# Optimization experiments

Measured on AMD Instinct MI355X. Metric: run time of the kernel, lower is better.

Reference implementation:

```python
import jax, jax.numpy as jnp
import numpy as np

B, N_PER, H, EMB, V, S, L = 128, 205, 200, 768, 50265, 512, 6
N = B * N_PER

def conv1d(x, w, b, pad):
    # x: [B, Cin, L], w: [Cout, Cin, K]
    out = jax.lax.conv_general_dilated(x, w, (1,), [(pad, pad)],
                                       dimension_numbers=('NCH', 'OIH', 'NCH'))
    return out + b[None, :, None]

def setup_inputs() -> dict:
    key = jax.random.key(0)
    ks = jax.random.split(key, 24)
    s = lambda fan: 1.0 / np.sqrt(fan)
    inp = {
        'x': jax.random.normal(ks[0], (N, H), jnp.float32),
        'edge_index': jax.random.randint(ks[1], (2, 209920), 0, N, jnp.int32),
        'input_ids': jax.random.randint(ks[2], (B, S), 0, V, jnp.int32),
        'embed_table': jax.random.normal(ks[3], (V, EMB), jnp.float32) * 0.02,
        'ggc_w': jax.random.normal(ks[4], (L, H, H), jnp.float32) * s(H),
        'gru_wih': jax.random.normal(ks[5], (3 * H, H), jnp.float32) * s(H),
        'gru_whh': jax.random.normal(ks[6], (3 * H, H), jnp.float32) * s(H),
        'gru_bih': jnp.zeros((3 * H,), jnp.float32),
        'gru_bhh': jnp.zeros((3 * H,), jnp.float32),
        'conv0_w': jax.random.normal(ks[7], (200, 200, 3), jnp.float32) * s(200 * 3),
        'conv0_b': jnp.zeros((200,), jnp.float32),
        'conv1_w': jax.random.normal(ks[8], (200, EMB, 3), jnp.float32) * s(EMB * 3),
        'conv1_b': jnp.zeros((200,), jnp.float32),
        'conv2_w': jax.random.normal(ks[9], (200, EMB, 4), jnp.float32) * s(EMB * 4),
        'conv2_b': jnp.zeros((200,), jnp.float32),
        'conv3_w': jax.random.normal(ks[10], (200, EMB, 5), jnp.float32) * s(EMB * 5),
        'conv3_b': jnp.zeros((200,), jnp.float32),
        'fc1_w': jax.random.normal(ks[11], (256, 800), jnp.float32) * s(800),
        'fc1_b': jnp.zeros((256,), jnp.float32),
        'fc2_w': jax.random.normal(ks[12], (128, 256), jnp.float32) * s(256),
        'fc2_b': jnp.zeros((128,), jnp.float32),
        'fc3_w': jax.random.normal(ks[13], (2, 128), jnp.float32) * s(128),
        'fc3_b': jnp.zeros((2,), jnp.float32),
    }
    return inp

def gated_graph_conv(x, edge_index, ggc_w, wih, whh, bih, bhh):
    src, dst = edge_index[0], edge_index[1]
    h = x  # [N, H], in_dim == out_channels so no padding needed
    for i in range(L):
        m = h @ ggc_w[i]                                   # [N, H]
        agg = jax.ops.segment_sum(m[src], dst, num_segments=N)  # scatter-add at targets
        gi = agg @ wih.T + bih                             # [N, 3H]
        gh = h @ whh.T + bhh
        ir, iz, inn = jnp.split(gi, 3, axis=1)
        hr, hz, hn = jnp.split(gh, 3, axis=1)
        r = jax.nn.sigmoid(ir + hr)
        z = jax.nn.sigmoid(iz + hz)
        n = jnp.tanh(inn + r * hn)
        h = (1.0 - z) * n + z * h
    return h

def reference(x, edge_index, input_ids, embed_table, ggc_w, gru_wih, gru_whh,
              gru_bih, gru_bhh, conv0_w, conv0_b, conv1_w, conv1_b, conv2_w,
              conv2_b, conv3_w, conv3_b, fc1_w, fc1_b, fc2_w, fc2_b, fc3_w, fc3_b):
    g = gated_graph_conv(x, edge_index, ggc_w, gru_wih, gru_whh, gru_bih, gru_bhh)
    g = g.reshape(B, N_PER, H).transpose(0, 2, 1)          # [B, 200, N_PER]
    e = embed_table[input_ids].transpose(0, 2, 1)          # [B, 768, S]
    x0 = jax.nn.relu(conv1d(g, conv0_w, conv0_b, 1))
    x1 = jax.nn.relu(conv1d(e, conv1_w, conv1_b, 0))
    x2 = jax.nn.relu(conv1d(e, conv2_w, conv2_b, 0))
    x3 = jax.nn.relu(conv1d(e, conv3_w, conv3_b, 0))
    feats = jnp.concatenate([x0.max(axis=2), x1.max(axis=2),
                             x2.max(axis=2), x3.max(axis=2)], axis=1)  # [B, 800]
    h = jax.nn.relu(feats @ fc1_w.T + fc1_b)   # dropout is identity in eval
    h = jax.nn.relu(h @ fc2_w.T + fc2_b)
    return h @ fc3_w.T + fc3_b                 # [B, 2]
```

## Files before the change

kernel.cpp:

```cpp
#include <hip/hip_runtime.h>
#include <math.h>

namespace {

constexpr int NB    = 128;
constexpr int NPER  = 205;
constexpr int H     = 200;
constexpr int EMBD  = 768;
constexpr int SEQ   = 512;
constexpr int NLAY  = 6;
constexpr int NNODE = NB * NPER;
constexpr int NEDGE = 209920;

typedef __bf16 bf16;
typedef _Float16 f16;
typedef __attribute__((ext_vector_type(8))) __bf16 bf16x8;
typedef __attribute__((ext_vector_type(8))) _Float16 f16x8;
typedef __attribute__((ext_vector_type(4))) float f32x4;
typedef unsigned short ushort8 __attribute__((ext_vector_type(8)));
typedef float float4v __attribute__((ext_vector_type(4)));

__device__ __forceinline__ float sigm(float x) { return 1.0f / (1.0f + expf(-x)); }

__device__ __forceinline__ unsigned short f2bf(float x) {
    unsigned int u = __float_as_uint(x);
    unsigned int r = (u + 0x7fffu + ((u >> 16) & 1u)) >> 16;
    return (unsigned short)r;
}
__device__ __forceinline__ unsigned short f2h(float x) {
    union { f16 h; unsigned short u; } c;
    c.h = (f16)x;
    return c.u;
}
__device__ __forceinline__ float h2f(unsigned short u) {
    union { unsigned short u; f16 h; } c;
    c.u = u;
    return (float)c.h;
}

__device__ __forceinline__ int pk_unit(int row, int s) {
    int q = row >> 1;
    return q * 8 + ((((row & 1) << 2) | s) ^ (q & 7));
}

template<bool BIAS, bool OUTF16>
__global__ __launch_bounds__(256, 4)
void gemm_w64(const unsigned short* __restrict__ A, int lda,
              const unsigned short* __restrict__ B,
              const float* __restrict__ bias, int Mreal, int Nreal,
              float* __restrict__ Cf, unsigned short* __restrict__ Ch,
              int ldc, int Kpad)
{
    __shared__ unsigned short As[128 * 64];
    __shared__ unsigned short Bs[128 * 64];

    const int p0 = blockIdx.x * 128;
    const int o0 = blockIdx.y * 128;
    const int tid = threadIdx.x, lane = tid & 63, wid = tid >> 6;
    const int wm = wid >> 1, wn = wid & 1;
    const int lrow = lane & 15, lk = lane >> 4;

    f32x4 acc[4][4];
    #pragma unroll
    for (int i = 0; i < 4; ++i)
        #pragma unroll
        for (int j = 0; j < 4; ++j) acc[i][j] = (f32x4){0.f, 0.f, 0.f, 0.f};

    for (int c0 = 0; c0 < Kpad; c0 += 64) {
        __syncthreads();
        for (int i = wid; i < 32; i += 4) {
            if (i < 16) {
                int u = i * 64 + lane;
                int row = u >> 3, slot = u & 7;
                int ss = slot ^ (row & 7);
                const unsigned short* sA = A + (size_t)(p0 + row) * lda + c0 + ss * 8;
                __builtin_amdgcn_global_load_lds(
                    (const __attribute__((address_space(1))) void*)sA,
                    (__attribute__((address_space(3))) void*)(As + i * 512), 16, 0, 0);
            } else {
                int i2 = i - 16;
                int u = i2 * 64 + lane;
                int row = u >> 3, slot = u & 7;
                int ss = slot ^ (row & 7);
                const unsigned short* sB = B + (size_t)(o0 + row) * Kpad + c0 + ss * 8;
                __builtin_amdgcn_global_load_lds(
                    (const __attribute__((address_space(1))) void*)sB,
                    (__attribute__((address_space(3))) void*)(Bs + i2 * 512), 16, 0, 0);
            }
        }
        __syncthreads();
        #pragma unroll
        for (int hf = 0; hf < 2; ++hf) {
            f16x8 vb[4];
            #pragma unroll
            for (int fn = 0; fn < 4; ++fn) {
                int r = wn * 64 + fn * 16 + lrow;
                int sl = (hf * 4 + lk) ^ (r & 7);
                vb[fn] = *reinterpret_cast<const f16x8*>(&Bs[r * 64 + sl * 8]);
            }
            #pragma unroll
            for (int fm = 0; fm < 4; ++fm) {
                int r = wm * 64 + fm * 16 + lrow;
                int sl = (hf * 4 + lk) ^ (r & 7);
                f16x8 va = *reinterpret_cast<const f16x8*>(&As[r * 64 + sl * 8]);
                #pragma unroll
                for (int fn = 0; fn < 4; ++fn)
                    acc[fm][fn] = __builtin_amdgcn_mfma_f32_16x16x32_f16(va, vb[fn], acc[fm][fn], 0, 0, 0);
            }
        }
    }
    #pragma unroll
    for (int fn = 0; fn < 4; ++fn) {
        int o = o0 + wn * 64 + fn * 16 + lrow;
        if (o >= Nreal) continue;
        float bv = BIAS ? bias[o] : 0.0f;
        #pragma unroll
        for (int fm = 0; fm < 4; ++fm) {
            #pragma unroll
            for (int i = 0; i < 4; ++i) {
                int p = p0 + wm * 64 + fm * 16 + lk * 4 + i;
                if (p >= Mreal) continue;
                float v = acc[fm][fn][i] + bv;
                if (OUTF16) Ch[(size_t)p * ldc + o] = f2h(v);
                else        Cf[(size_t)p * ldc + o] = v;
            }
        }
    }
}

template<int K, int CINP, int LIN, int LOUT>
__global__ __launch_bounds__(512, 4)
void conv_w64(const unsigned short* __restrict__ E, const unsigned short* __restrict__ WT,
              const float* __restrict__ bias, int COUT,
              float* __restrict__ feats, int foff)
{
    constexpr int AROWS  = 272;
    constexpr int AINSTR = AROWS * 4 / 64;
    constexpr int BINSTR = K * 128 * 4 / 64;
    __shared__ unsigned short As[AROWS * 32];
    __shared__ unsigned short Bs[K * 128 * 32];

    const int p0 = blockIdx.x * 256;
    const int o0 = blockIdx.y * 128;
    const int b  = blockIdx.z;
    const int tid = threadIdx.x, lane = tid & 63, wid = tid >> 6;
    const int wm = wid >> 1, wn = wid & 1;
    const int lrow = lane & 15, lk = lane >> 4;

    const unsigned short* Eb = E + (size_t)b * LIN * CINP;

    f32x4 acc[4][4];
    #pragma unroll
    for (int i = 0; i < 4; ++i)
        #pragma unroll
        for (int j = 0; j < 4; ++j) acc[i][j] = (f32x4){0.f, 0.f, 0.f, 0.f};

    for (int c0 = 0; c0 < CINP; c0 += 32) {
        __syncthreads();
        for (int i = wid; i < AINSTR + BINSTR; i += 8) {
            if (i < AINSTR) {
                int u = i * 64 + lane;
                int q = u >> 3, cs = u & 7;
                int bs = cs ^ (q & 7);
                int row = q * 2 + (bs >> 2), s = bs & 3;
                int srow = p0 + row; if (srow > LIN - 1) srow = LIN - 1;
                const unsigned short* src = Eb + (size_t)srow * CINP + c0 + s * 8;
                __builtin_amdgcn_global_load_lds(
                    (const __attribute__((address_space(1))) void*)src,
                    (__attribute__((address_space(3))) void*)(As + i * 512), 16, 0, 0);
            } else {
                int i2 = i - AINSTR;
                int u = i2 * 64 + lane;
                int q = u >> 3, cs = u & 7;
                int bs = cs ^ (q & 7);
                int R = q * 2 + (bs >> 2), s = bs & 3;
                int k = R >> 7, r = R & 127;
                const unsigned short* src = WT + ((size_t)k * 256 + o0 + r) * CINP + c0 + s * 8;
                __builtin_amdgcn_global_load_lds(
                    (const __attribute__((address_space(1))) void*)src,
                    (__attribute__((address_space(3))) void*)(Bs + i2 * 512), 16, 0, 0);
            }
        }
        __syncthreads();
        #pragma unroll
        for (int k = 0; k < K; ++k) {
            bf16x8 vb[4];
            #pragma unroll
            for (int fn = 0; fn < 4; ++fn) {
                int R = k * 128 + wn * 64 + fn * 16 + lrow;
                vb[fn] = *reinterpret_cast<const bf16x8*>(&Bs[pk_unit(R, lk) * 8]);
            }
            #pragma unroll
            for (int fm = 0; fm < 4; ++fm) {
                int r = wm * 64 + fm * 16 + lrow + k;
                bf16x8 va = *reinterpret_cast<const bf16x8*>(&As[pk_unit(r, lk) * 8]);
                #pragma unroll
                for (int fn = 0; fn < 4; ++fn)
                    acc[fm][fn] = __builtin_amdgcn_mfma_f32_16x16x32_bf16(va, vb[fn], acc[fm][fn], 0, 0, 0);
            }
        }
    }
    #pragma unroll
    for (int fn = 0; fn < 4; ++fn) {
        int o = o0 + wn * 64 + fn * 16 + lrow;
        float mx = 0.0f;
        if (o < COUT) {
            float bv = bias[o];
            #pragma unroll
            for (int fm = 0; fm < 4; ++fm)
                #pragma unroll
                for (int i = 0; i < 4; ++i) {
                    int p = p0 + wm * 64 + fm * 16 + lk * 4 + i;
                    if (p < LOUT) mx = fmaxf(mx, acc[fm][fn][i] + bv);
                }
        }
        mx = fmaxf(mx, __shfl_xor(mx, 16));
        mx = fmaxf(mx, __shfl_xor(mx, 32));
        if (lane < 16 && o < COUT)
            atomicMax((int*)&feats[(size_t)b * 800 + foff + o], __float_as_int(mx));
    }
}

__global__ void hist_kernel(const int* __restrict__ dst, int* __restrict__ deg)
{
    int e = blockIdx.x * 256 + threadIdx.x;
    if (e < NEDGE) atomicAdd(&deg[dst[e]], 1);
}

__global__ void scan_kernel(const int* __restrict__ deg, int* __restrict__ off, int* __restrict__ cur)
{
    __shared__ int part[1024];
    const int tid = threadIdx.x;
    const int CH = (NNODE + 1023) / 1024;
    int base = tid * CH;
    int s = 0;
    for (int i = 0; i < CH; ++i) { int idx = base + i; s += (idx < NNODE ? deg[idx] : 0); }
    part[tid] = s;
    __syncthreads();
    for (int d = 1; d < 1024; d <<= 1) {
        int v = (tid >= d) ? part[tid - d] : 0;
        __syncthreads();
        part[tid] += v;
        __syncthreads();
    }
    int run = tid ? part[tid - 1] : 0;
    for (int i = 0; i < CH; ++i) {
        int idx = base + i;
        if (idx < NNODE) { off[idx] = run; cur[idx] = run; run += deg[idx]; }
    }
    if (tid == 1023) off[NNODE] = run;
}

__global__ void fill_kernel(const int* __restrict__ src, const int* __restrict__ dst,
                            int* __restrict__ cur, int* __restrict__ eidx)
{
    int e = blockIdx.x * 256 + threadIdx.x;
    if (e >= NEDGE) return;
    int d = dst[e];
    int pos = atomicAdd(&cur[d], 1);
    eidx[pos] = src[e];
}

__global__ void gather_h2(const int* __restrict__ off, const int* __restrict__ eidx,
                          unsigned short* __restrict__ acat)
{
    int t = blockIdx.x * 256 + threadIdx.x;
    if (t >= NNODE * 32) return;
    int c8 = t & 31, n = t >> 5;
    float s[8] = {0.f, 0.f, 0.f, 0.f, 0.f, 0.f, 0.f, 0.f};
    if (c8 < 25) {
        const size_t cb = (size_t)c8 * 8;
        int beg = off[n], end = off[n + 1];
        for (int i = beg; i < end; ++i) {
            int sn = eidx[i];
            ushort8 hh = *(const ushort8*)(acat + (size_t)sn * 512 + 256 + cb);
            #pragma unroll
            for (int j = 0; j < 8; ++j) s[j] += h2f(hh[j]);
        }
    }
    ushort8 o;
    #pragma unroll
    for (int j = 0; j < 8; ++j) o[j] = f2h(s[j]);
    *(ushort8*)(acat + (size_t)n * 512 + c8 * 8) = o;
}

__global__ void gru2_kernel(const unsigned short* __restrict__ S, unsigned short* __restrict__ acat)
{
    int gid = blockIdx.x * 256 + threadIdx.x;
    if (gid >= NNODE * H) return;
    int n = gid / H, c = gid % H;
    const unsigned short* Sn = S + (size_t)n * 896;
    float r = sigm(h2f(Sn[c]));
    float z = sigm(h2f(Sn[200 + c]));
    float nn = tanhf(h2f(Sn[400 + c]) + r * h2f(Sn[600 + c]));
    size_t hidx = (size_t)n * 512 + 256 + c;
    float h_old = h2f(acat[hidx]);
    acat[hidx] = f2h((1.0f - z) * nn + z * h_old);
}

__global__ void h0_kernel(const float* __restrict__ x, unsigned short* __restrict__ acat)
{
    int t = blockIdx.x * 256 + threadIdx.x;
    if (t >= NNODE * 32) return;
    int c8 = t & 31, n = t >> 5;
    ushort8 o = {0,0,0,0,0,0,0,0};
    if (c8 < 25) {
        const float* src = x + (size_t)n * H + c8 * 8;
        float4v v0 = *(const float4v*)src;
        float4v v1 = *(const float4v*)(src + 4);
        o[0] = f2h(v0[0]); o[1] = f2h(v0[1]); o[2] = f2h(v0[2]); o[3] = f2h(v0[3]);
        o[4] = f2h(v1[0]); o[5] = f2h(v1[1]); o[6] = f2h(v1[2]); o[7] = f2h(v1[3]);
    }
    *(ushort8*)(acat + (size_t)n * 512 + 256 + c8 * 8) = o;
}

__global__ void wih16_prep(const float* __restrict__ wih, unsigned short* __restrict__ w16)
{
    int t = blockIdx.x * 256 + threadIdx.x;
    if (t >= 640 * 32) return;
    int c8 = t & 31, r = t >> 5;
    ushort8 o = {0,0,0,0,0,0,0,0};
    if (r < 600) {
        #pragma unroll
        for (int j = 0; j < 8; ++j) {
            int k = c8 * 8 + j;
            if (k < H) o[j] = f2h(wih[(size_t)r * H + k]);
        }
    }
    *(ushort8*)(w16 + (size_t)r * 256 + c8 * 8) = o;
}

__global__ void wl_prep(const float* __restrict__ w, unsigned short* __restrict__ wl)
{
    int t = blockIdx.x * 256 + threadIdx.x;
    if (t >= NLAY * 256 * 32) return;
    int c8 = t & 31;
    int rest = t >> 5;
    int jr = rest & 255;
    int l = rest >> 8;
    ushort8 o = {0,0,0,0,0,0,0,0};
    if (jr < H) {
        #pragma unroll
        for (int j = 0; j < 8; ++j) {
            int k = c8 * 8 + j;
            if (k < H) o[j] = f2h(w[(size_t)l * H * H + (size_t)jr * H + k]);
        }
    }
    *(ushort8*)(wl + (size_t)l * 65536 + (size_t)jr * 256 + c8 * 8) = o;
}

__global__ void wf_right(const float* __restrict__ whh, const float* __restrict__ bih,
                         const float* __restrict__ bhh,
                         unsigned short* __restrict__ Wf, float* __restrict__ bb)
{
    int t = blockIdx.x * 256 + threadIdx.x;
    if (t >= NLAY * 896 * 32) return;
    int c8 = t & 31;
    int rest = t >> 5;
    int r = rest % 896;
    int l = rest / 896;
    ushort8 o = {0,0,0,0,0,0,0,0};
    #pragma unroll
    for (int j = 0; j < 8; ++j) {
        int kk = c8 * 8 + j;
        float v = 0.0f;
        if (kk < H) {
            if (r < 400) v = whh[(size_t)r * H + kk];
            else if (r >= 600 && r < 800) v = whh[(size_t)(r - 200) * H + kk];
        }
        o[j] = f2h(v);
    }
    *(ushort8*)(Wf + (size_t)l * 458752 + (size_t)r * 512 + 256 + c8 * 8) = o;
    if (l == 0 && c8 == 0) {
        float bv = 0.0f;
        if (r < 400) bv = bih[r] + bhh[r];
        else if (r < 600) bv = bih[r];
        else if (r < 800) bv = bhh[r - 200];
        bb[r] = bv;
    }
}

__global__ void embed_bf16_kernel(const int* __restrict__ ids, const float* __restrict__ table,
                                  unsigned short* __restrict__ e)
{
    int t = blockIdx.x * 256 + threadIdx.x;
    const int total = NB * SEQ * (EMBD / 8);
    if (t >= total) return;
    int j = t % (EMBD / 8), row = t / (EMBD / 8);
    int id = ids[row];
    const float* src = table + (size_t)id * EMBD + j * 8;
    float4v v0 = *(const float4v*)src;
    float4v v1 = *(const float4v*)(src + 4);
    ushort8 o;
    o[0] = f2bf(v0[0]); o[1] = f2bf(v0[1]); o[2] = f2bf(v0[2]); o[3] = f2bf(v0[3]);
    o[4] = f2bf(v1[0]); o[5] = f2bf(v1[1]); o[6] = f2bf(v1[2]); o[7] = f2bf(v1[3]);
    *(ushort8*)(e + (size_t)row * EMBD + j * 8) = o;
}

__global__ void h_pad_from_acat(const unsigned short* __restrict__ acat,
                                unsigned short* __restrict__ e0)
{
    int t = blockIdx.x * 256 + threadIdx.x;
    const int total = NB * 208 * 32;
    if (t >= total) return;
    int c8 = t % 32, rest = t / 32;
    int r = rest % 208, b = rest / 208;
    ushort8 o = {0,0,0,0,0,0,0,0};
    if (r >= 1 && r <= 205) {
        int node = b * NPER + (r - 1);
        ushort8 hh = *(const ushort8*)(acat + (size_t)node * 512 + 256 + c8 * 8);
        #pragma unroll
        for (int j = 0; j < 8; ++j) o[j] = f2bf(h2f(hh[j]));
    }
    *(ushort8*)(e0 + ((size_t)(b * 208 + r)) * 256 + c8 * 8) = o;
}

__global__ void wconv_bf16_kernel(const float* __restrict__ w, unsigned short* __restrict__ wt,
                                  int K, int CINP, int CINR, int COUT)
{
    long long t = (long long)blockIdx.x * 256 + threadIdx.x;
    long long total = (long long)K * 256 * CINP;
    if (t >= total) return;
    int cin = (int)(t % CINP);
    long long rest = t / CINP;
    int o = (int)(rest % 256), k = (int)(rest / 256);
    float v = 0.0f;
    if (o < COUT && cin < CINR) v = w[((size_t)o * CINR + cin) * K + k];
    wt[t] = f2bf(v);
}

__global__ __launch_bounds__(256)
void fc_head(const float* __restrict__ feats,
             const float* __restrict__ w1, const float* __restrict__ b1,
             const float* __restrict__ w2, const float* __restrict__ b2,
             const float* __restrict__ w3, const float* __restrict__ b3,
             float* __restrict__ out)
{
    __shared__ float f[800];
    __shared__ float h1[256];
    __shared__ float h2[128];
    const int b = blockIdx.x, tid = threadIdx.x;
    for (int i = tid; i < 800; i += 256) f[i] = feats[(size_t)b * 800 + i];
    __syncthreads();
    {
        float acc = b1[tid];
        const float* wr = w1 + (size_t)tid * 800;
        for (int k = 0; k < 800; ++k) acc = fmaf(f[k], wr[k], acc);
        h1[tid] = fmaxf(acc, 0.0f);
    }
    __syncthreads();
    if (tid < 128) {
        float acc = b2[tid];
        const float* wr = w2 + (size_t)tid * 256;
        for (int k = 0; k < 256; ++k) acc = fmaf(h1[k], wr[k], acc);
        h2[tid] = fmaxf(acc, 0.0f);
    }
    __syncthreads();
    if (tid < 2) {
        float acc = b3[tid];
        const float* wr = w3 + (size_t)tid * 128;
        for (int k = 0; k < 128; ++k) acc = fmaf(h2[k], wr[k], acc);
        out[(size_t)b * 2 + tid] = acc;
    }
}

}

extern "C" void kernel_launch(void* const* d_in, const int* in_sizes, int n_in,
                              void* d_out, int out_size, void* d_ws, size_t ws_size,
                              hipStream_t stream)
{
    const float* x         = (const float*)d_in[0];
    const int*   edge      = (const int*)d_in[1];
    const int*   input_ids = (const int*)d_in[2];
    const float* table     = (const float*)d_in[3];
    const float* ggc_w     = (const float*)d_in[4];
    const float* wih       = (const float*)d_in[5];
    const float* whh       = (const float*)d_in[6];
    const float* bih       = (const float*)d_in[7];
    const float* bhh       = (const float*)d_in[8];
    const float* c0w = (const float*)d_in[9];  const float* c0b = (const float*)d_in[10];
    const float* c1w = (const float*)d_in[11]; const float* c1b = (const float*)d_in[12];
    const float* c2w = (const float*)d_in[13]; const float* c2b = (const float*)d_in[14];
    const float* c3w = (const float*)d_in[15]; const float* c3b = (const float*)d_in[16];
    const float* f1w = (const float*)d_in[17]; const float* f1b = (const float*)d_in[18];
    const float* f2w = (const float*)d_in[19]; const float* f2b = (const float*)d_in[20];
    const float* f3w = (const float*)d_in[21]; const float* f3b = (const float*)d_in[22];
    float* out = (float*)d_out;

    float* ws = (float*)d_ws;
    unsigned short* acat  = (unsigned short*)(ws + 0);
    unsigned short* S16   = (unsigned short*)(ws + 6717440);
    unsigned short* Wf    = (unsigned short*)(ws + 18472960);
    unsigned short* wl16  = (unsigned short*)(ws + 19849216);
    unsigned short* wih16 = (unsigned short*)(ws + 20045824);
    float* b_big = ws + 20127744;
    int* deg  = (int*)(ws + 20128640);
    int* off  = (int*)(ws + 20154880);
    int* cur  = (int*)(ws + 20181121);
    int* eidx = (int*)(ws + 20207362);
    unsigned short* e_bf16 = (unsigned short*)(ws + 0);
    unsigned short* e0     = (unsigned short*)(ws + 25165824);
    unsigned short* wt0    = (unsigned short*)(ws + 28600000);
    unsigned short* wt1    = wt0 + (size_t)3 * 256 * 256;
    unsigned short* wt2    = wt1 + (size_t)3 * 256 * EMBD;
    unsigned short* wt3    = wt2 + (size_t)4 * 256 * EMBD;
    float* feats = ws + 29900000;

    const int* srcp = edge;
    const int* dstp = edge + NEDGE;

    dim3 blk(256);
    dim3 blk512(512);

    hipMemsetAsync(deg, 0, sizeof(int) * NNODE, stream);
    hist_kernel<<<dim3((NEDGE + 255) / 256), blk, 0, stream>>>(dstp, deg);
    scan_kernel<<<dim3(1), dim3(1024), 0, stream>>>(deg, off, cur);
    fill_kernel<<<dim3((NEDGE + 255) / 256), blk, 0, stream>>>(srcp, dstp, cur, eidx);
    h0_kernel<<<dim3((NNODE * 32 + 255) / 256), blk, 0, stream>>>(x, acat);
    wih16_prep<<<dim3((640 * 32 + 255) / 256), blk, 0, stream>>>(wih, wih16);
    wl_prep<<<dim3((NLAY * 256 * 32 + 255) / 256), blk, 0, stream>>>(ggc_w, wl16);
    hipMemsetAsync(Wf, 0, (size_t)NLAY * 896 * 512 * 2, stream);
    wf_right<<<dim3((NLAY * 896 * 32 + 255) / 256), blk, 0, stream>>>(whh, bih, bhh, Wf, b_big);
    for (int l = 0; l < NLAY; ++l) {
        gemm_w64<false, true><<<dim3(5, 2), blk, 0, stream>>>(
            wih16, 256, wl16 + (size_t)l * 65536, nullptr, 640, 200,
            nullptr, Wf + (size_t)l * 458752, 512, 256);
    }

    for (int l = 0; l < NLAY; ++l) {
        gather_h2<<<dim3((NNODE * 32 + 255) / 256), blk, 0, stream>>>(off, eidx, acat);
        gemm_w64<true, true><<<dim3(NNODE / 128, 7), blk, 0, stream>>>(
            acat, 512, Wf + (size_t)l * 458752, b_big, NNODE, 800,
            nullptr, S16, 896, 512);
        gru2_kernel<<<dim3((NNODE * H + 255) / 256), blk, 0, stream>>>(S16, acat);
    }

    h_pad_from_acat<<<dim3((NB * 208 * 32 + 255) / 256), blk, 0, stream>>>(acat, e0);
    embed_bf16_kernel<<<dim3(NB * SEQ * (EMBD / 8) / 256), blk, 0, stream>>>(input_ids, table, e_bf16);
    wconv_bf16_kernel<<<dim3((3 * 256 * 256 + 255) / 256), blk, 0, stream>>>(c0w, wt0, 3, 256, 200, 200);
    wconv_bf16_kernel<<<dim3((3 * 256 * EMBD + 255) / 256), blk, 0, stream>>>(c1w, wt1, 3, EMBD, EMBD, 200);
    wconv_bf16_kernel<<<dim3((4 * 256 * EMBD + 255) / 256), blk, 0, stream>>>(c2w, wt2, 4, EMBD, EMBD, 200);
    wconv_bf16_kernel<<<dim3((5 * 256 * EMBD + 255) / 256), blk, 0, stream>>>(c3w, wt3, 5, EMBD, EMBD, 200);

    hipMemsetAsync(feats, 0, sizeof(float) * NB * 800, stream);
    conv_w64<3, 256, 208, 205><<<dim3(1, 2, NB), blk512, 0, stream>>>(e0, wt0, c0b, 200, feats, 0);
    conv_w64<3, EMBD, SEQ, 510><<<dim3(2, 2, NB), blk512, 0, stream>>>(e_bf16, wt1, c1b, 200, feats, 200);
    conv_w64<4, EMBD, SEQ, 509><<<dim3(2, 2, NB), blk512, 0, stream>>>(e_bf16, wt2, c2b, 200, feats, 400);
    conv_w64<5, EMBD, SEQ, 508><<<dim3(2, 2, NB), blk512, 0, stream>>>(e_bf16, wt3, c3b, 200, feats, 600);

    fc_head<<<dim3(NB), blk, 0, stream>>>(feats, f1w, f1b, f2w, f2b, f3w, f3b, out);
}
```

Before: 1.092 ms.

## Fuse GRU gate epilogue into GGC GEMM and double-buffer conv LDS staging

```diff
diff --git a/kernel.cpp b/kernel.cpp
--- a/kernel.cpp
+++ b/kernel.cpp
@@ -128,8 +128,107 @@
     }
 }
 
+__global__ __launch_bounds__(256, 2)
+void gemm_gru(const unsigned short* __restrict__ A,
+              const unsigned short* __restrict__ B,
+              const float* __restrict__ bb,
+              unsigned short* __restrict__ Hn)
+{
+    __shared__ unsigned short As[2][128 * 64];
+    __shared__ unsigned short Bs[2][128 * 64];
+
+    const int p0 = blockIdx.x * 128;
+    const int o0 = blockIdx.y * 128;
+    const int tid = threadIdx.x, lane = tid & 63, wid = tid >> 6;
+    const int wm = wid >> 1, wn = wid & 1;
+    const int lrow = lane & 15, lk = lane >> 4;
+
+    auto stage = [&](int bs, int c0) {
+        for (int i = wid; i < 32; i += 4) {
+            if (i < 16) {
+                int u = i * 64 + lane;
+                int row = u >> 3, slot = u & 7;
+                int ss = slot ^ (row & 7);
+                const unsigned short* sA = A + (size_t)(p0 + row) * 512 + c0 + ss * 8;
+                __builtin_amdgcn_global_load_lds(
+                    (const __attribute__((address_space(1))) void*)sA,
+                    (__attribute__((address_space(3))) void*)(&As[bs][i * 512]), 16, 0, 0);
+            } else {
+                int i2 = i - 16;
+                int u = i2 * 64 + lane;
+                int row = u >> 3, slot = u & 7;
+                int ss = slot ^ (row & 7);
+                const unsigned short* sB = B + (size_t)(o0 + row) * 512 + c0 + ss * 8;
+                __builtin_amdgcn_global_load_lds(
+                    (const __attribute__((address_space(1))) void*)sB,
+                    (__attribute__((address_space(3))) void*)(&Bs[bs][i2 * 512]), 16, 0, 0);
+            }
+        }
+    };
+
+    f32x4 acc[4][4];
+    #pragma unroll
+    for (int i = 0; i < 4; ++i)
+        #pragma unroll
+        for (int j = 0; j < 4; ++j) acc[i][j] = (f32x4){0.f, 0.f, 0.f, 0.f};
+
+    stage(0, 0);
+    __syncthreads();
+    int bs = 0;
+    for (int t = 0; t < 8; ++t) {
+        if (t + 1 < 8) stage(bs ^ 1, (t + 1) * 64);
+        const unsigned short* Asc = As[bs];
+        const unsigned short* Bsc = Bs[bs];
+        #pragma unroll
+        for (int hf = 0; hf < 2; ++hf) {
+            f16x8 vb[4];
+            #pragma unroll
+            for (int fn = 0; fn < 4; ++fn) {
+                int r = wn * 64 + fn * 16 + lrow;
+                int sl = (hf * 4 + lk) ^ (r & 7);
+                vb[fn] = *reinterpret_cast<const f16x8*>(&Bsc[r * 64 + sl * 8]);
+            }
+            #pragma unroll
+            for (int fm = 0; fm < 4; ++fm) {
+                int r = wm * 64 + fm * 16 + lrow;
+                int sl = (hf * 4 + lk) ^ (r & 7);
+                f16x8 va = *reinterpret_cast<const f16x8*>(&Asc[r * 64 + sl * 8]);
+                #pragma unroll
+                for (int fn = 0; fn < 4; ++fn)
+                    acc[fm][fn] = __builtin_amdgcn_mfma_f32_16x16x32_f16(va, vb[fn], acc[fm][fn], 0, 0, 0);
+            }
+        }
+        __syncthreads();
+        bs ^= 1;
+    }
+
+    const int colbase = o0 + wn * 64;
+    const int c = (colbase >> 2) + lrow;
+    float b0 = bb[colbase + 0 * 16 + lrow];
+    float b1 = bb[colbase + 1 * 16 + lrow];
+    float b2 = bb[colbase + 2 * 16 + lrow];
+    float b3 = bb[colbase + 3 * 16 + lrow];
+    #pragma unroll
+    for (int fm = 0; fm < 4; ++fm) {
+        #pragma unroll
+        for (int i = 0; i < 4; ++i) {
+            int p = p0 + wm * 64 + fm * 16 + lk * 4 + i;
+            size_t hidx = (size_t)p * 512 + 256 + c;
+            if (c < H) {
+                float r = sigm(acc[fm][0][i] + b0);
+                float z = sigm(acc[fm][1][i] + b1);
+                float nn = tanhf((acc[fm][2][i] + b2) + r * (acc[fm][3][i] + b3));
+                float ho = h2f(A[hidx]);
+                Hn[hidx] = f2h((1.0f - z) * nn + z * ho);
+            } else {
+                Hn[hidx] = 0;
+            }
+        }
+    }
+}
+
 template<int K, int CINP, int LIN, int LOUT>
-__global__ __launch_bounds__(512, 4)
+__global__ __launch_bounds__(512, 1)
 void conv_w64(const unsigned short* __restrict__ E, const unsigned short* __restrict__ WT,
               const float* __restrict__ bias, int COUT,
               float* __restrict__ feats, int foff)
@@ -137,8 +236,8 @@
     constexpr int AROWS  = 272;
     constexpr int AINSTR = AROWS * 4 / 64;
     constexpr int BINSTR = K * 128 * 4 / 64;
-    __shared__ unsigned short As[AROWS * 32];
-    __shared__ unsigned short Bs[K * 128 * 32];
+    __shared__ unsigned short As[2][AROWS * 32];
+    __shared__ unsigned short Bs[2][K * 128 * 32];
 
     const int p0 = blockIdx.x * 256;
     const int o0 = blockIdx.y * 128;
@@ -149,56 +248,66 @@
 
     const unsigned short* Eb = E + (size_t)b * LIN * CINP;
 
-    f32x4 acc[4][4];
-    #pragma unroll
-    for (int i = 0; i < 4; ++i)
-        #pragma unroll
-        for (int j = 0; j < 4; ++j) acc[i][j] = (f32x4){0.f, 0.f, 0.f, 0.f};
-
-    for (int c0 = 0; c0 < CINP; c0 += 32) {
-        __syncthreads();
+    auto stage = [&](int bsl, int c0) {
         for (int i = wid; i < AINSTR + BINSTR; i += 8) {
             if (i < AINSTR) {
                 int u = i * 64 + lane;
                 int q = u >> 3, cs = u & 7;
-                int bs = cs ^ (q & 7);
-                int row = q * 2 + (bs >> 2), s = bs & 3;
+                int bsw = cs ^ (q & 7);
+                int row = q * 2 + (bsw >> 2), s = bsw & 3;
                 int srow = p0 + row; if (srow > LIN - 1) srow = LIN - 1;
                 const unsigned short* src = Eb + (size_t)srow * CINP + c0 + s * 8;
                 __builtin_amdgcn_global_load_lds(
                     (const __attribute__((address_space(1))) void*)src,
-                    (__attribute__((address_space(3))) void*)(As + i * 512), 16, 0, 0);
+                    (__attribute__((address_space(3))) void*)(&As[bsl][i * 512]), 16, 0, 0);
             } else {
                 int i2 = i - AINSTR;
                 int u = i2 * 64 + lane;
                 int q = u >> 3, cs = u & 7;
-                int bs = cs ^ (q & 7);
-                int R = q * 2 + (bs >> 2), s = bs & 3;
+                int bsw = cs ^ (q & 7);
+                int R = q * 2 + (bsw >> 2), s = bsw & 3;
                 int k = R >> 7, r = R & 127;
                 const unsigned short* src = WT + ((size_t)k * 256 + o0 + r) * CINP + c0 + s * 8;
                 __builtin_amdgcn_global_load_lds(
                     (const __attribute__((address_space(1))) void*)src,
-                    (__attribute__((address_space(3))) void*)(Bs + i2 * 512), 16, 0, 0);
-            }
-        }
-        __syncthreads();
+                    (__attribute__((address_space(3))) void*)(&Bs[bsl][i2 * 512]), 16, 0, 0);
+            }
+        }
+    };
+
+    f32x4 acc[4][4];
+    #pragma unroll
+    for (int i = 0; i < 4; ++i)
+        #pragma unroll
+        for (int j = 0; j < 4; ++j) acc[i][j] = (f32x4){0.f, 0.f, 0.f, 0.f};
+
+    stage(0, 0);
+    __syncthreads();
+    constexpr int nit = CINP / 32;
+    int bsl = 0;
+    for (int t = 0; t < nit; ++t) {
+        if (t + 1 < nit) stage(bsl ^ 1, (t + 1) * 32);
+        const unsigned short* Asc = As[bsl];
+        const unsigned short* Bsc = Bs[bsl];
         #pragma unroll
         for (int k = 0; k < K; ++k) {
             bf16x8 vb[4];
             #pragma unroll
             for (int fn = 0; fn < 4; ++fn) {
                 int R = k * 128 + wn * 64 + fn * 16 + lrow;
-                vb[fn] = *reinterpret_cast<const bf16x8*>(&Bs[pk_unit(R, lk) * 8]);
+                vb[fn] = *reinterpret_cast<const bf16x8*>(&Bsc[pk_unit(R, lk) * 8]);
             }
             #pragma unroll
             for (int fm = 0; fm < 4; ++fm) {
                 int r = wm * 64 + fm * 16 + lrow + k;
-                bf16x8 va = *reinterpret_cast<const bf16x8*>(&As[pk_unit(r, lk) * 8]);
+                bf16x8 va = *reinterpret_cast<const bf16x8*>(&Asc[pk_unit(r, lk) * 8]);
                 #pragma unroll
                 for (int fn = 0; fn < 4; ++fn)
                     acc[fm][fn] = __builtin_amdgcn_mfma_f32_16x16x32_bf16(va, vb[fn], acc[fm][fn], 0, 0, 0);
             }
         }
+        __syncthreads();
+        bsl ^= 1;
     }
     #pragma unroll
     for (int fn = 0; fn < 4; ++fn) {
@@ -284,20 +393,6 @@
     *(ushort8*)(acat + (size_t)n * 512 + c8 * 8) = o;
 }
 
-__global__ void gru2_kernel(const unsigned short* __restrict__ S, unsigned short* __restrict__ acat)
-{
-    int gid = blockIdx.x * 256 + threadIdx.x;
-    if (gid >= NNODE * H) return;
-    int n = gid / H, c = gid % H;
-    const unsigned short* Sn = S + (size_t)n * 896;
-    float r = sigm(h2f(Sn[c]));
-    float z = sigm(h2f(Sn[200 + c]));
-    float nn = tanhf(h2f(Sn[400 + c]) + r * h2f(Sn[600 + c]));
-    size_t hidx = (size_t)n * 512 + 256 + c;
-    float h_old = h2f(acat[hidx]);
-    acat[hidx] = f2h((1.0f - z) * nn + z * h_old);
-}
-
 __global__ void h0_kernel(const float* __restrict__ x, unsigned short* __restrict__ acat)
 {
     int t = blockIdx.x * 256 + threadIdx.x;
@@ -314,17 +409,19 @@
     *(ushort8*)(acat + (size_t)n * 512 + 256 + c8 * 8) = o;
 }
 
-__global__ void wih16_prep(const float* __restrict__ wih, unsigned short* __restrict__ w16)
+__global__ void wih16p_prep(const float* __restrict__ wih, unsigned short* __restrict__ w16)
 {
     int t = blockIdx.x * 256 + threadIdx.x;
-    if (t >= 640 * 32) return;
+    if (t >= 896 * 32) return;
     int c8 = t & 31, r = t >> 5;
+    int g = (r >> 4) & 3;
+    int c = (r >> 6) * 16 + (r & 15);
     ushort8 o = {0,0,0,0,0,0,0,0};
-    if (r < 600) {
+    if (g < 3 && c < H) {
         #pragma unroll
         for (int j = 0; j < 8; ++j) {
             int k = c8 * 8 + j;
-            if (k < H) o[j] = f2h(wih[(size_t)r * H + k]);
+            if (k < H) o[j] = f2h(wih[(size_t)(g * 200 + c) * H + k]);
         }
     }
     *(ushort8*)(w16 + (size_t)r * 256 + c8 * 8) = o;
@@ -349,9 +446,9 @@
     *(ushort8*)(wl + (size_t)l * 65536 + (size_t)jr * 256 + c8 * 8) = o;
 }
 
-__global__ void wf_right(const float* __restrict__ whh, const float* __restrict__ bih,
-                         const float* __restrict__ bhh,
-                         unsigned short* __restrict__ Wf, float* __restrict__ bb)
+__global__ void wf_rightp(const float* __restrict__ whh, const float* __restrict__ bih,
+                          const float* __restrict__ bhh,
+                          unsigned short* __restrict__ Wf, float* __restrict__ bb)
 {
     int t = blockIdx.x * 256 + threadIdx.x;
     if (t >= NLAY * 896 * 32) return;
@@ -359,23 +456,31 @@
     int rest = t >> 5;
     int r = rest % 896;
     int l = rest / 896;
+    int g = (r >> 4) & 3;
+    int c = (r >> 6) * 16 + (r & 15);
     ushort8 o = {0,0,0,0,0,0,0,0};
-    #pragma unroll
-    for (int j = 0; j < 8; ++j) {
-        int kk = c8 * 8 + j;
-        float v = 0.0f;
-        if (kk < H) {
-            if (r < 400) v = whh[(size_t)r * H + kk];
-            else if (r >= 600 && r < 800) v = whh[(size_t)(r - 200) * H + kk];
-        }
-        o[j] = f2h(v);
+    if (c < H) {
+        #pragma unroll
+        for (int j = 0; j < 8; ++j) {
+            int kk = c8 * 8 + j;
+            float v = 0.0f;
+            if (kk < H) {
+                if (g == 0)      v = whh[(size_t)c * H + kk];
+                else if (g == 1) v = whh[(size_t)(200 + c) * H + kk];
+                else if (g == 3) v = whh[(size_t)(400 + c) * H + kk];
+            }
+            o[j] = f2h(v);
+        }
     }
     *(ushort8*)(Wf + (size_t)l * 458752 + (size_t)r * 512 + 256 + c8 * 8) = o;
     if (l == 0 && c8 == 0) {
         float bv = 0.0f;
-        if (r < 400) bv = bih[r] + bhh[r];
-        else if (r < 600) bv = bih[r];
-        else if (r < 800) bv = bhh[r - 200];
+        if (c < H) {
+            if (g == 0)      bv = bih[c] + bhh[c];
+            else if (g == 1) bv = bih[200 + c] + bhh[200 + c];
+            else if (g == 2) bv = bih[400 + c];
+            else             bv = bhh[400 + c];
+        }
         bb[r] = bv;
     }
 }
@@ -489,16 +594,16 @@
     float* out = (float*)d_out;
 
     float* ws = (float*)d_ws;
-    unsigned short* acat  = (unsigned short*)(ws + 0);
-    unsigned short* S16   = (unsigned short*)(ws + 6717440);
-    unsigned short* Wf    = (unsigned short*)(ws + 18472960);
-    unsigned short* wl16  = (unsigned short*)(ws + 19849216);
-    unsigned short* wih16 = (unsigned short*)(ws + 20045824);
-    float* b_big = ws + 20127744;
-    int* deg  = (int*)(ws + 20128640);
-    int* off  = (int*)(ws + 20154880);
-    int* cur  = (int*)(ws + 20181121);
-    int* eidx = (int*)(ws + 20207362);
+    unsigned short* acat_a = (unsigned short*)(ws + 0);
+    unsigned short* acat_b = (unsigned short*)(ws + 6717440);
+    unsigned short* Wf     = (unsigned short*)(ws + 13434880);
+    unsigned short* wl16   = (unsigned short*)(ws + 14811136);
+    unsigned short* wih16p = (unsigned short*)(ws + 15007744);
+    float* b_big = ws + 15122432;
+    int* deg  = (int*)(ws + 15123328);
+    int* off  = (int*)(ws + 15149568);
+    int* cur  = (int*)(ws + 15175809);
+    int* eidx = (int*)(ws + 15202050);
     unsigned short* e_bf16 = (unsigned short*)(ws + 0);
     unsigned short* e0     = (unsigned short*)(ws + 25165824);
     unsigned short* wt0    = (unsigned short*)(ws + 28600000);
@@ -517,26 +622,27 @@
     hist_kernel<<<dim3((NEDGE + 255) / 256), blk, 0, stream>>>(dstp, deg);
     scan_kernel<<<dim3(1), dim3(1024), 0, stream>>>(deg, off, cur);
     fill_kernel<<<dim3((NEDGE + 255) / 256), blk, 0, stream>>>(srcp, dstp, cur, eidx);
-    h0_kernel<<<dim3((NNODE * 32 + 255) / 256), blk, 0, stream>>>(x, acat);
-    wih16_prep<<<dim3((640 * 32 + 255) / 256), blk, 0, stream>>>(wih, wih16);
+    h0_kernel<<<dim3((NNODE * 32 + 255) / 256), blk, 0, stream>>>(x, acat_a);
+    wih16p_prep<<<dim3((896 * 32 + 255) / 256), blk, 0, stream>>>(wih, wih16p);
     wl_prep<<<dim3((NLAY * 256 * 32 + 255) / 256), blk, 0, stream>>>(ggc_w, wl16);
     hipMemsetAsync(Wf, 0, (size_t)NLAY * 896 * 512 * 2, stream);
-    wf_right<<<dim3((NLAY * 896 * 32 + 255) / 256), blk, 0, stream>>>(whh, bih, bhh, Wf, b_big);
+    wf_rightp<<<dim3((NLAY * 896 * 32 + 255) / 256), blk, 0, stream>>>(whh, bih, bhh, Wf, b_big);
     for (int l = 0; l < NLAY; ++l) {
-        gemm_w64<false, true><<<dim3(5, 2), blk, 0, stream>>>(
-            wih16, 256, wl16 + (size_t)l * 65536, nullptr, 640, 200,
+        gemm_w64<false, true><<<dim3(7, 2), blk, 0, stream>>>(
+            wih16p, 256, wl16 + (size_t)l * 65536, nullptr, 896, 200,
             nullptr, Wf + (size_t)l * 458752, 512, 256);
     }
 
+    unsigned short* bufs[2] = { acat_a, acat_b };
     for (int l = 0; l < NLAY; ++l) {
-        gather_h2<<<dim3((NNODE * 32 + 255) / 256), blk, 0, stream>>>(off, eidx, acat);
-        gemm_w64<true, true><<<dim3(NNODE / 128, 7), blk, 0, stream>>>(
-            acat, 512, Wf + (size_t)l * 458752, b_big, NNODE, 800,
-            nullptr, S16, 896, 512);
-        gru2_kernel<<<dim3((NNODE * H + 255) / 256), blk, 0, stream>>>(S16, acat);
-    }
-
-    h_pad_from_acat<<<dim3((NB * 208 * 32 + 255) / 256), blk, 0, stream>>>(acat, e0);
+        unsigned short* curb = bufs[l & 1];
+        unsigned short* nxtb = bufs[(l + 1) & 1];
+        gather_h2<<<dim3((NNODE * 32 + 255) / 256), blk, 0, stream>>>(off, eidx, curb);
+        gemm_gru<<<dim3(NNODE / 128, 7), blk, 0, stream>>>(
+            curb, Wf + (size_t)l * 458752, b_big, nxtb);
+    }
+
+    h_pad_from_acat<<<dim3((NB * 208 * 32 + 255) / 256), blk, 0, stream>>>(acat_a, e0);
     embed_bf16_kernel<<<dim3(NB * SEQ * (EMBD / 8) / 256), blk, 0, stream>>>(input_ids, table, e_bf16);
     wconv_bf16_kernel<<<dim3((3 * 256 * 256 + 255) / 256), blk, 0, stream>>>(c0w, wt0, 3, 256, 200, 200);
     wconv_bf16_kernel<<<dim3((3 * 256 * EMBD + 255) / 256), blk, 0, stream>>>(c1w, wt1, 3, EMBD, EMBD, 200);
```

Measured after the change: 1.086 ms. No clear change (-0.5%).
